# Kernel optimization log

Measured on AMD Instinct MI355X. Metric: run time of the kernel, lower is better.

Reference implementation:

```python
import jax, jax.numpy as jnp
import numpy as np

N, C, T, V = 64, 64, 128, 25
OUT, REL = 64, 8
MID = OUT // 2
BN_EPS = 1e-5


def _conv1x1(x, w, b):
    # 1x1 Conv2d: x [n,c,h,w_], w [o,c], b [o]
    return jnp.einsum('nchw,oc->nohw', x, w) + b[None, :, None, None]


def _forward(x, A, w1, b1, w2, b2, w11, b11, w22, b22, w3, b3, w4, b4,
             watt, batt, w5, b5, wc1, bc1, bn_g, bn_b, bn_m, bn_v,
             wc2, bc2, ws, bs, beita, alpha):
    T_ = x.shape[2]
    rel = w1.shape[0]
    x1 = _conv1x1(x, w1, b1)                          # [N,rel,T,V]
    x2 = _conv1x1(x, w2, b2)
    x1_mean, x2_mean = x1.mean(2), x2.mean(2)         # [N,rel,V]
    x1_max, x2_max = x1.max(2), x2.max(2)
    mean_res = x1_mean[:, :, :, None] - x2_mean[:, :, None, :]   # [N,rel,V,V]
    max_res = x1_max[:, :, :, None] - x2_max[:, :, None, :]
    # conv5: grouped 1x1 conv (groups=rel, 2 in-ch/group). The cat(dim=2)+reshape
    # interleaves channels as (mean[c], max[c]) pairs, so per-group it is:
    x_1 = jnp.tanh(w5[None, :, 0, None, None] * mean_res
                   + w5[None, :, 1, None, None] * max_res
                   + b5[None, :, None, None]) * alpha
    x_1 = _conv1x1(x_1, w4, b4)                       # [N,out,V,V]
    x3 = _conv1x1(x, w3, b3)                          # [N,out,T,V]
    x1_res = x_1 + A[None, None]
    # channel-wise spatial correlation attention
    att = jnp.tanh(jnp.einsum('nctu,nctv->ncuv', x1, x2) / T_)
    att = _conv1x1(att, watt, batt)                   # [N,out,V,V]
    global_res = jnp.einsum('nctu,ncuv->nctv', x3, att)
    # Bi_Inter 'channel': global avg pool -> 1x1 -> BN(inference) -> GELU -> 1x1 -> sigmoid
    g = global_res.mean((2, 3), keepdims=True)        # [N,out,1,1]
    h = _conv1x1(g, wc1, bc1)
    h = (h - bn_m[None, :, None, None]) * (bn_g[None, :, None, None]
        / jnp.sqrt(bn_v[None, :, None, None] + BN_EPS)) + bn_b[None, :, None, None]
    h = jax.nn.gelu(h, approximate=False)
    c_att = jax.nn.sigmoid(_conv1x1(h, wc2, bc2))     # [N,out,1,1]
    x1_res = c_att * x1_res
    x1_res = jnp.einsum('ncuv,nctv->nctu', x1_res, x3)  # [N,out,T,V]
    # Bi_Inter 'spatial': mean over T -> 1x1 (out->1) -> sigmoid
    s_att = jax.nn.sigmoid(_conv1x1(x1_res.mean(2, keepdims=True), ws, bs))  # [N,1,1,V]
    global_res = global_res * s_att
    x1_res = x1_res + global_res
    # per-frame spatial correlation (temporal branch)
    x11 = _conv1x1(x, w11, b11)
    x22 = _conv1x1(x, w22, b22)
    xt = jnp.tanh(jnp.einsum('nctv,nctu->ntvu', x11, x22) / rel)  # [N,T,V,V]
    t_res = jnp.einsum('nctu,ntuv->nctv', x3, xt)
    return t_res * beita + x1_res                     # [N,out,T,V]


def setup_inputs() -> dict:
    key = jax.random.key(0)
    ks = jax.random.split(key, 16)
    def nrm(i, shape, s=0.05):
        return jax.random.normal(ks[i], shape, jnp.float32) * s
    return {
        'x': jax.random.normal(ks[0], (N, C, T, V), jnp.float32),
        'A': nrm(1, (V, V), 0.1),
        'w1': nrm(2, (REL, C)), 'b1': jnp.zeros((REL,), jnp.float32),
        'w2': nrm(3, (REL, C)), 'b2': jnp.zeros((REL,), jnp.float32),
        'w11': nrm(4, (REL, C)), 'b11': jnp.zeros((REL,), jnp.float32),
        'w22': nrm(5, (REL, C)), 'b22': jnp.zeros((REL,), jnp.float32),
        'w3': nrm(6, (OUT, C)), 'b3': jnp.zeros((OUT,), jnp.float32),
        'w4': nrm(7, (OUT, REL)), 'b4': jnp.zeros((OUT,), jnp.float32),
        'watt': nrm(8, (OUT, REL)), 'batt': jnp.zeros((OUT,), jnp.float32),
        'w5': nrm(9, (REL, 2)), 'b5': jnp.zeros((REL,), jnp.float32),
        'wc1': nrm(10, (MID, OUT)), 'bc1': jnp.zeros((MID,), jnp.float32),
        'bn_g': jnp.ones((MID,), jnp.float32), 'bn_b': jnp.zeros((MID,), jnp.float32),
        'bn_m': jnp.zeros((MID,), jnp.float32), 'bn_v': jnp.ones((MID,), jnp.float32),
        'wc2': nrm(11, (OUT, MID)), 'bc2': jnp.zeros((OUT,), jnp.float32),
        'ws': nrm(12, (1, OUT)), 'bs': jnp.zeros((1,), jnp.float32),
        'beita': jnp.full((1,), 0.5, jnp.float32),
        'alpha': 1,
    }


def reference(x, A, w1, b1, w2, b2, w11, b11, w22, b22, w3, b3, w4, b4,
              watt, batt, w5, b5, wc1, bc1, bn_g, bn_b, bn_m, bn_v,
              wc2, bc2, ws, bs, beita, alpha):
    return _forward(x, A, w1, b1, w2, b2, w11, b11, w22, b22, w3, b3, w4, b4,
                    watt, batt, w5, b5, wc1, bc1, bn_g, bn_b, bn_m, bn_v,
                    wc2, bc2, ws, bs, beita, alpha)
```

## Files before the change

kernel.cpp:

```cpp
#include <hip/hip_runtime.h>
#include <hip/hip_bf16.h>
#include <math.h>

#define N_   64
#define C_   64
#define T_   128
#define V_   25
#define OUT_ 64
#define REL_ 8
#define MID_ 32
#define TV_  (T_*V_)
#define VV_  (V_*V_)
#define TT2  8
#define XTPF 28

typedef __hip_bfloat16 bf16;
typedef unsigned int uint;
typedef __attribute__((ext_vector_type(8))) short short8v;
typedef __attribute__((ext_vector_type(4))) float float4v;
__device__ __forceinline__ float b2f(bf16 x){ return __bfloat162float(x); }
__device__ __forceinline__ bf16  f2b(float x){ return __float2bfloat16(x); }
__device__ __forceinline__ float bfu(uint u){ return __uint_as_float(u<<16); }
__device__ __forceinline__ float bfh(uint u){ return __uint_as_float(u&0xffff0000u); }
__device__ __forceinline__ float bfs(unsigned short s){ return __uint_as_float(((uint)s)<<16); }

__device__ __forceinline__ float ftanh(float x){
    float cx = fminf(fmaxf(x, -15.f), 15.f);
    float e  = __expf(2.0f*cx);
    return (e - 1.0f) / (e + 1.0f);
}


__global__ __launch_bounds__(256) void k0_prep(
    const float* __restrict__ w1, const float* __restrict__ b1,
    const float* __restrict__ w2, const float* __restrict__ b2,
    const float* __restrict__ w11, const float* __restrict__ b11,
    const float* __restrict__ w22, const float* __restrict__ b22,
    const float* __restrict__ w3, const float* __restrict__ b3,
    unsigned short* __restrict__ WfragUS, float* __restrict__ Bg)
{
    int tid = threadIdx.x;
    for (int idx = tid; idx < 6144; idx += 256){
        int e  = idx & 7;
        int ln = (idx >> 3) & 63;
        int kb = (idx >> 9) & 1;
        int mt = idx >> 10;
        int m = mt*16 + (ln & 15);
        int k = kb*32 + ((ln >> 4) * 8) + e;
        float w;
        if      (m < 8)  w = w1[m*C_+k];
        else if (m < 16) w = w2[(m-8)*C_+k];
        else if (m < 24) w = w11[(m-16)*C_+k];
        else if (m < 32) w = w22[(m-24)*C_+k];
        else             w = w3[(m-32)*C_+k];
        bf16 h = f2b(w);
        WfragUS[idx] = *(unsigned short*)&h;
    }
    if (tid < 96){
        int o = tid; float bb;
        if      (o < 8)  bb = b1[o];
        else if (o < 16) bb = b2[o-8];
        else if (o < 24) bb = b11[o-16];
        else if (o < 32) bb = b22[o-24];
        else             bb = b3[o-32];
        Bg[o] = bb;
    }
}

__global__ __launch_bounds__(256) void k1_mfma(
    const float* __restrict__ x,
    const unsigned short* __restrict__ WfragUS, const float* __restrict__ Bg,
    bf16* __restrict__ x1h, bf16* __restrict__ x2h,
    bf16* __restrict__ x11h, bf16* __restrict__ x22h,
    bf16* __restrict__ x3h)
{
    __shared__ __align__(16) float xl[C_*64];
    __shared__ float Bl[96];
    int bid = blockIdx.x;
    int n = bid / 50, jt = bid % 50;
    int j0 = jt * 64;
    int tid = threadIdx.x;
    for (int e = tid; e < 1024; e += 256){
        int c = e >> 4, j4 = e & 15;
        ((float4*)xl)[e] = ((const float4*)(x + (size_t)(n*C_+c)*TV_ + j0))[j4];
    }
    if (tid < 96) Bl[tid] = Bg[tid];
    __syncthreads();

    int wave = tid >> 6, lane = tid & 63;
    int l15 = lane & 15, lg = lane >> 4;
    const short8v* wf = (const short8v*)WfragUS;
    short8v a[6][2];
    #pragma unroll
    for (int mt = 0; mt < 6; ++mt)
        #pragma unroll
        for (int kb = 0; kb < 2; ++kb)
            a[mt][kb] = wf[(mt*2 + kb)*64 + lane];
    int jw = wave*16 + l15;
    short8v b[2];
    #pragma unroll
    for (int kb = 0; kb < 2; ++kb){
        short8v bb;
        #pragma unroll
        for (int e = 0; e < 8; ++e){
            bf16 h = f2b(xl[(kb*32 + lg*8 + e)*64 + jw]);
            bb[e] = *(short*)&h;
        }
        b[kb] = bb;
    }
    float4v acc[6];
    #pragma unroll
    for (int mt = 0; mt < 6; ++mt) acc[mt] = (float4v){0.f,0.f,0.f,0.f};
    #pragma unroll
    for (int kb = 0; kb < 2; ++kb)
        #pragma unroll
        for (int mt = 0; mt < 6; ++mt)
            acc[mt] = __builtin_amdgcn_mfma_f32_16x16x32_bf16(a[mt][kb], b[kb], acc[mt], 0, 0, 0);

    int pos = j0 + jw;
    #pragma unroll
    for (int mt = 0; mt < 6; ++mt){
        #pragma unroll
        for (int reg = 0; reg < 4; ++reg){
            int o = mt*16 + lg*4 + reg;
            float val = acc[mt][reg] + Bl[o];
            bf16* dst = (o < 8)  ? x1h  + ((size_t)(n*REL_ + o     ))*TV_
                      : (o < 16) ? x2h  + ((size_t)(n*REL_ + o - 8 ))*TV_
                      : (o < 24) ? x11h + ((size_t)(n*REL_ + o - 16))*TV_
                      : (o < 32) ? x22h + ((size_t)(n*REL_ + o - 24))*TV_
                                 : x3h  + ((size_t)(n*OUT_ + o - 32))*TV_;
            dst[pos] = f2b(val);
        }
    }
}

__global__ __launch_bounds__(256) void k_x3bar2(const bf16* __restrict__ x3h,
                                                float* __restrict__ x3bar)
{
    __shared__ __align__(16) float xf[TV_];
    __shared__ float red[V_*8];
    int bid = blockIdx.x;
    int tid = threadIdx.x;
    for (int e = tid; e < 400; e += 256){
        uint4 p = ((const uint4*)(x3h + (size_t)bid*TV_))[e];
        float* d = xf + e*8;
        d[0]=bfu(p.x); d[1]=bfh(p.x); d[2]=bfu(p.y); d[3]=bfh(p.y);
        d[4]=bfu(p.z); d[5]=bfh(p.z); d[6]=bfu(p.w); d[7]=bfh(p.w);
    }
    __syncthreads();
    if (tid < 200){
        int v = tid % V_, g = tid / V_;
        float s = 0.f;
        #pragma unroll
        for (int k=0;k<16;++k) s += xf[(g*16+k)*V_ + v];
        red[g*V_+v] = s;
    }
    __syncthreads();
    if (tid < V_){
        float s = 0.f;
        #pragma unroll
        for (int g=0; g<8; ++g) s += red[g*V_+tid];
        x3bar[(size_t)bid*V_+tid] = s * (1.0f/T_);
    }
}

__global__ __launch_bounds__(256) void k3_mfma(
    const bf16* __restrict__ x1h, const bf16* __restrict__ x2h,
    const float* __restrict__ w5, const float* __restrict__ b5,
    const int* __restrict__ alpha,
    float* __restrict__ att8, float* __restrict__ xm)
{
    __shared__ __align__(16) unsigned short l1[TV_], l2[TV_];
    __shared__ float mu1l[V_], mu2l[V_], m1l[V_], m2l[V_];
    int bid = blockIdx.x;
    int tid = threadIdx.x;
    int r = bid % REL_;
    for (int e = tid; e < 400; e += 256){
        ((uint4*)l1)[e] = ((const uint4*)(x1h + (size_t)bid*TV_))[e];
        ((uint4*)l2)[e] = ((const uint4*)(x2h + (size_t)bid*TV_))[e];
    }
    __syncthreads();
    if (tid < 50){
        int v = tid % V_;
        const unsigned short* L = (tid < V_) ? l1 : l2;
        float s=0.f, mm=-1e30f;
        for (int t=0;t<T_;++t){
            float a = bfs(L[t*V_+v]);
            s += a; mm = fmaxf(mm, a);
        }
        if (tid < V_){ mu1l[v]=s*(1.0f/T_); m1l[v]=mm; }
        else         { mu2l[v]=s*(1.0f/T_); m2l[v]=mm; }
    }
    __syncthreads();
    int wave = tid >> 6, lane = tid & 63;
    int l15 = lane & 15, lg = lane >> 4;
    int mt = wave >> 1, nt = wave & 1;
    int mu = mt*16 + l15;
    int nv = nt*16 + l15;
    float4v acc = (float4v){0.f,0.f,0.f,0.f};
    #pragma unroll
    for (int kb = 0; kb < 4; ++kb){
        short8v av, bv;
        #pragma unroll
        for (int e = 0; e < 8; ++e){
            int k = kb*32 + lg*8 + e;
            av[e] = (mu < V_) ? (short)l1[k*V_ + mu] : (short)0;
            bv[e] = (nv < V_) ? (short)l2[k*V_ + nv] : (short)0;
        }
        acc = __builtin_amdgcn_mfma_f32_16x16x32_bf16(av, bv, acc, 0, 0, 0);
    }
    #pragma unroll
    for (int reg = 0; reg < 4; ++reg){
        int u = mt*16 + lg*4 + reg;
        if (u < V_ && nv < V_)
            att8[(size_t)bid*VV_ + u*V_ + nv] = ftanh(acc[reg]*(1.0f/T_));
    }
    float w50=w5[r*2+0], w51=w5[r*2+1], b5r=b5[r];
    float af = (float)alpha[0];
    for (int idx=tid; idx<VV_; idx+=256){
        int u = idx/V_, v = idx%V_;
        float mr = mu1l[u]-mu2l[v];
        float xr = m1l[u]-m2l[v];
        xm[(size_t)bid*VV_+idx] = ftanh(fmaf(w50,mr,fmaf(w51,xr,b5r))) * af;
    }
}

__global__ __launch_bounds__(256) void k6_chatt2(
    const float* __restrict__ att8, const float* __restrict__ x3bar,
    const float* __restrict__ watt, const float* __restrict__ batt,
    const float* __restrict__ wc1, const float* __restrict__ bc1,
    const float* __restrict__ bng, const float* __restrict__ bnb,
    const float* __restrict__ bnm, const float* __restrict__ bnv,
    const float* __restrict__ wc2, const float* __restrict__ bc2,
    float* __restrict__ catt)
{
    __shared__ float rs8[REL_*V_];
    __shared__ float gl[OUT_];
    __shared__ float hl[MID_];
    int n = blockIdx.x, tid = threadIdx.x;
    if (tid < REL_*V_){
        int r = tid / V_, u = tid % V_;
        const float* p = att8 + (size_t)(n*REL_+r)*VV_ + u*V_;
        float s = 0.f;
        #pragma unroll
        for (int v=0;v<V_;++v) s += p[v];
        rs8[tid] = s;
    }
    __syncthreads();
    if (tid < OUT_){
        int c = tid;
        const float* xb = x3bar + (size_t)(n*OUT_+c)*V_;
        float xbr[V_], sb = 0.f;
        #pragma unroll
        for (int u=0;u<V_;++u){ xbr[u]=xb[u]; sb += xbr[u]; }
        float s = 0.f;
        #pragma unroll
        for (int r=0;r<REL_;++r){
            float d = 0.f;
            #pragma unroll
            for (int u=0;u<V_;++u) d = fmaf(xbr[u], rs8[r*V_+u], d);
            s = fmaf(watt[c*REL_+r], d, s);
        }
        gl[c] = (s + (float)V_*batt[c]*sb) * (1.0f/(float)V_);
    }
    __syncthreads();
    if (tid < MID_){
        float h = bc1[tid];
        for (int c=0;c<OUT_;++c) h = fmaf(wc1[tid*OUT_+c], gl[c], h);
        h = (h - bnm[tid]) * bng[tid] * rsqrtf(bnv[tid] + 1e-5f) + bnb[tid];
        h = 0.5f*h*(1.0f+erff(h*0.70710678118654752f));
        hl[tid]=h;
    }
    __syncthreads();
    if (tid < OUT_){
        float s = bc2[tid];
        for (int m=0;m<MID_;++m) s = fmaf(wc2[tid*MID_+m], hl[m], s);
        catt[n*OUT_+tid] = 1.0f/(1.0f+expf(-s));
    }
}

__global__ __launch_bounds__(256) void k8_satt3(
    const float* __restrict__ xm, const float* __restrict__ A,
    const float* __restrict__ catt, const float* __restrict__ x3bar,
    const float* __restrict__ w4, const float* __restrict__ b4,
    const float* __restrict__ wsp, const float* __restrict__ bsp,
    float* __restrict__ satt)
{
    __shared__ __align__(16) float xml[REL_*VV_];
    __shared__ __align__(16) float xbl[OUT_*V_];
    __shared__ float Al[VV_];
    __shared__ float w4l[OUT_*REL_];
    __shared__ float scl[OUT_];
    __shared__ float Wl[REL_*V_];
    __shared__ float Yl[V_];
    __shared__ float red[OUT_];
    int n = blockIdx.x, tid = threadIdx.x;
    for (int e=tid; e<1250; e+=256)
        ((float4*)xml)[e] = ((const float4*)(xm + (size_t)n*REL_*VV_))[e];
    for (int e=tid; e<400; e+=256)
        ((float4*)xbl)[e] = ((const float4*)(x3bar + (size_t)n*OUT_*V_))[e];
    for (int e=tid; e<VV_; e+=256) Al[e] = A[e];
    for (int e=tid; e<OUT_*REL_; e+=256) w4l[e] = w4[e];
    if (tid < OUT_) scl[tid] = wsp[tid]*catt[n*OUT_+tid];
    __syncthreads();
    if (tid < REL_*V_){
        int r = tid/V_, v = tid%V_;
        float s = 0.f;
        for (int c=0;c<OUT_;++c) s = fmaf(scl[c]*w4l[c*REL_+r], xbl[c*V_+v], s);
        Wl[tid] = s;
    } else if (tid < REL_*V_ + V_){
        int v = tid - REL_*V_;
        float s = 0.f;
        for (int c=0;c<OUT_;++c) s = fmaf(scl[c], xbl[c*V_+v], s);
        Yl[v] = s;
    }
    __syncthreads();
    if (tid < OUT_){
        float s1 = 0.f;
        #pragma unroll
        for (int v=0;v<V_;++v) s1 += xbl[tid*V_+v];
        red[tid] = scl[tid]*b4[tid]*s1;
    }
    __syncthreads();
    if (tid < V_){
        int u = tid;
        float acc = 0.f;
        #pragma unroll
        for (int r=0;r<REL_;++r){
            const float* xr = xml + r*VV_ + u*V_;
            const float* wr = Wl + r*V_;
            #pragma unroll
            for (int v=0;v<V_;++v) acc = fmaf(xr[v], wr[v], acc);
        }
        #pragma unroll
        for (int v=0;v<V_;++v) acc = fmaf(Al[u*V_+v], Yl[v], acc);
        float beta = 0.f;
        for (int c=0;c<OUT_;++c) beta += red[c];
        satt[n*V_+u] = 1.0f/(1.0f+expf(-(bsp[0]+acc+beta)));
    }
}

__global__ __launch_bounds__(256) void k_comb3(
    const bf16* __restrict__ x3h,
    const float* __restrict__ att8, const float* __restrict__ xm,
    const float* __restrict__ A,
    const float* __restrict__ watt, const float* __restrict__ batt,
    const float* __restrict__ w4, const float* __restrict__ b4,
    const float* __restrict__ catt, const float* __restrict__ satt,
    bf16* __restrict__ combh)
{
    __shared__ __align__(16) unsigned short x3s[TV_];
    __shared__ float Ml[VV_];
    __shared__ float sl[V_];
    __shared__ __align__(16) unsigned short cst[TV_];
    int bid = blockIdx.x;
    int n = bid >> 6, c = bid & 63;
    int tid = threadIdx.x;
    for (int e = tid; e < 400; e += 256)
        ((uint4*)x3s)[e] = ((const uint4*)(x3h + (size_t)bid*TV_))[e];
    if (tid < V_) sl[tid] = satt[n*V_+tid];
    float ca = catt[bid];
    float w4r[REL_], war[REL_];
    #pragma unroll
    for (int r=0;r<REL_;++r){ w4r[r] = w4[c*REL_+r]; war[r] = watt[c*REL_+r]; }
    float b4c = b4[c], bac = batt[c];
    const float* xmn = xm  + (size_t)n*REL_*VV_;
    const float* a8n = att8 + (size_t)n*REL_*VV_;
    __syncthreads();
    for (int e = tid; e < VV_; e += 256){
        int w = e/V_, u = e%V_;
        float xv = b4c, av = bac;
        #pragma unroll
        for (int r=0;r<REL_;++r){
            xv = fmaf(w4r[r], xmn[r*VV_ + e], xv);
            av = fmaf(war[r], a8n[r*VV_ + u*V_ + w], av);
        }
        Ml[e] = ca*(xv + A[e]) + av*sl[w];
    }
    __syncthreads();
    int vh = tid & 1, tq = tid >> 1;
    int v0 = vh*13, nv = vh ? 12 : 13;
    float x3r[V_];
    #pragma unroll
    for (int u=0;u<V_;++u) x3r[u] = bfs(x3s[tq*V_+u]);
    for (int i=0;i<nv;++i){
        int v = v0+i;
        float s=0.f;
        #pragma unroll
        for (int u=0;u<V_;++u) s = fmaf(Ml[v*V_+u], x3r[u], s);
        bf16 h = f2b(s);
        cst[tq*V_+v] = *(unsigned short*)&h;
    }
    __syncthreads();
    for (int e = tid; e < 400; e += 256)
        ((uint4*)(combh + (size_t)bid*TV_))[e] = ((const uint4*)cst)[e];
}

__global__ __launch_bounds__(512) void k10_final8(
    const bf16* __restrict__ x11h, const bf16* __restrict__ x22h,
    const bf16* __restrict__ x3h, const bf16* __restrict__ combh,
    const float* __restrict__ beita, float* __restrict__ out)
{
    __shared__ __align__(16) char stg[25600];
    __shared__ __align__(16) float xtl[TT2*V_*XTPF];
    int bid = blockIdx.x;
    int n = bid >> 4, tt = bid & 15;
    int t0 = tt * TT2;
    int tid = threadIdx.x;
    float* l11 = (float*)stg;
    float* l22 = (float*)(stg + 6400);
    for (int e = tid; e < 400; e += 512){
        int half = (e >= 200);
        int i = half ? e-200 : e;
        int r = i / 25, ch = i % 25;
        const bf16* src = (half ? x22h : x11h) + (size_t)(n*REL_+r)*TV_ + t0*V_ + ch*8;
        uint4 p = *(const uint4*)src;
        float* d = (half ? l22 : l11) + i*8;
        d[0]=bfu(p.x); d[1]=bfh(p.x); d[2]=bfu(p.y); d[3]=bfh(p.y);
        d[4]=bfu(p.z); d[5]=bfh(p.z); d[6]=bfu(p.w); d[7]=bfh(p.w);
    }
    __syncthreads();
    for (int e = tid; e < TT2*VV_; e += 512){
        int ti = e / VV_, uv = e % VV_;
        int u = uv / V_, v = uv % V_;
        float s = 0.f;
        #pragma unroll
        for (int r = 0; r < REL_; ++r)
            s = fmaf(l11[r*200 + ti*V_ + u], l22[r*200 + ti*V_ + v], s);
        xtl[ti*(V_*XTPF) + u*XTPF + v] = ftanh(s * 0.125f);
    }
    float bt = beita[0];
    int vh = tid >> 8;
    int c_local = (tid >> 3) & 31;
    int ti = tid & 7;
    int vbase = vh ? 12 : 0;
    int nvv   = vh ? 13 : 12;
    for (int cr = 0; cr < 2; ++cr){
        int c0 = cr*32;
        __syncthreads();
        for (int e = tid; e < 1600; e += 512){
            int cl = e / 50, w = e % 50;
            size_t base = (size_t)(n*OUT_ + c0 + cl)*TV_ + (size_t)t0*V_;
            uint4 p = (w < 25) ? ((const uint4*)(combh + base))[w]
                               : ((const uint4*)(x3h  + base))[w-25];
            *(uint4*)(stg + cl*800 + (w<25 ? w*16 : 400 + (w-25)*16)) = p;
        }
        __syncthreads();
        const unsigned short* x3row = (const unsigned short*)(stg + c_local*800 + 400) + ti*V_;
        float acc[13];
        #pragma unroll
        for (int j=0;j<13;++j) acc[j]=0.f;
        const float* xbase = xtl + ti*(V_*XTPF) + vbase;
        #pragma unroll
        for (int u=0;u<V_;++u){
            float xa = bfs(x3row[u]);
            const float* xr = xbase + u*XTPF;
            if (vh == 0){
                #pragma unroll
                for (int j=0;j<12;++j) acc[j] = fmaf(xa, xr[j], acc[j]);
            } else {
                #pragma unroll
                for (int j=0;j<13;++j) acc[j] = fmaf(xa, xr[j], acc[j]);
            }
        }
        const unsigned short* cmbrow =
            (const unsigned short*)(stg + c_local*800) + ti*V_ + vbase;
        if (vh == 0){
            #pragma unroll
            for (int j=0;j<12;++j) acc[j] = fmaf(bt, acc[j], bfs(cmbrow[j]));
        } else {
            #pragma unroll
            for (int j=0;j<13;++j) acc[j] = fmaf(bt, acc[j], bfs(cmbrow[j]));
        }
        __syncthreads();
        float* orow = (float*)(stg + c_local*800 + ti*100) + vbase;
        if (vh == 0){
            #pragma unroll
            for (int j=0;j<12;++j) orow[j] = acc[j];
        } else {
            #pragma unroll
            for (int j=0;j<13;++j) orow[j] = acc[j];
        }
        __syncthreads();
        for (int e = tid; e < 1600; e += 512){
            int cl = e / 50, q = e % 50;
            *(float4*)(out + (size_t)(n*OUT_ + c0 + cl)*TV_ + (size_t)t0*V_ + q*4) =
                *(const float4*)(stg + cl*800 + q*16);
        }
    }
}

extern "C" void kernel_launch(void* const* d_in, const int* in_sizes, int n_in,
                              void* d_out, int out_size, void* d_ws, size_t ws_size,
                              hipStream_t stream)
{
    const float* x    = (const float*)d_in[0];
    const float* A    = (const float*)d_in[1];
    const float* w1   = (const float*)d_in[2];  const float* b1  = (const float*)d_in[3];
    const float* w2   = (const float*)d_in[4];  const float* b2  = (const float*)d_in[5];
    const float* w11  = (const float*)d_in[6];  const float* b11 = (const float*)d_in[7];
    const float* w22  = (const float*)d_in[8];  const float* b22 = (const float*)d_in[9];
    const float* w3   = (const float*)d_in[10]; const float* b3  = (const float*)d_in[11];
    const float* w4   = (const float*)d_in[12]; const float* b4  = (const float*)d_in[13];
    const float* watt = (const float*)d_in[14]; const float* batt= (const float*)d_in[15];
    const float* w5   = (const float*)d_in[16]; const float* b5  = (const float*)d_in[17];
    const float* wc1  = (const float*)d_in[18]; const float* bc1 = (const float*)d_in[19];
    const float* bng  = (const float*)d_in[20]; const float* bnb = (const float*)d_in[21];
    const float* bnm  = (const float*)d_in[22]; const float* bnv = (const float*)d_in[23];
    const float* wc2  = (const float*)d_in[24]; const float* bc2 = (const float*)d_in[25];
    const float* wsp  = (const float*)d_in[26]; const float* bsp = (const float*)d_in[27];
    const float* beita= (const float*)d_in[28];
    const int*  alpha = (const int*)d_in[29];
    float* out = (float*)d_out;

    char* wsb = (char*)d_ws;
    size_t off = 0;
    auto alloc = [&](size_t bytes)->char*{
        char* p = wsb + off;
        off += (bytes + 255) & ~(size_t)255;
        return p;
    };
    bf16*  x1h   = (bf16*) alloc((size_t)N_*REL_*TV_*2);
    bf16*  x2h   = (bf16*) alloc((size_t)N_*REL_*TV_*2);
    bf16*  x11h  = (bf16*) alloc((size_t)N_*REL_*TV_*2);
    bf16*  x22h  = (bf16*) alloc((size_t)N_*REL_*TV_*2);
    bf16*  x3h   = (bf16*) alloc((size_t)N_*OUT_*TV_*2);
    bf16*  combh = (bf16*) alloc((size_t)N_*OUT_*TV_*2);
    float* att8  = (float*)alloc((size_t)N_*REL_*VV_*4);
    float* xm    = (float*)alloc((size_t)N_*REL_*VV_*4);
    float* x3bar = (float*)alloc((size_t)N_*OUT_*V_*4);
    float* catt  = (float*)alloc((size_t)N_*OUT_*4);
    float* satt  = (float*)alloc((size_t)N_*V_*4);
    unsigned short* WfragUS = (unsigned short*)alloc((size_t)6144*2);
    float* Bg    = (float*)alloc((size_t)96*4);
    (void)ws_size; (void)n_in; (void)in_sizes; (void)out_size;

    k0_prep<<<1, 256, 0, stream>>>(w1,b1, w2,b2, w11,b11, w22,b22, w3,b3, WfragUS, Bg);
    k1_mfma<<<N_*50, 256, 0, stream>>>(x, WfragUS, Bg, x1h, x2h, x11h, x22h, x3h);
    k_x3bar2<<<N_*OUT_, 256, 0, stream>>>(x3h, x3bar);
    k3_mfma<<<N_*REL_, 256, 0, stream>>>(x1h, x2h, w5, b5, alpha, att8, xm);
    k6_chatt2<<<N_, 256, 0, stream>>>(att8, x3bar, watt, batt,
                                      wc1, bc1, bng, bnb, bnm, bnv, wc2, bc2, catt);
    k8_satt3<<<N_, 256, 0, stream>>>(xm, A, catt, x3bar, w4, b4, wsp, bsp, satt);
    k_comb3<<<N_*OUT_, 256, 0, stream>>>(x3h, att8, xm, A, watt, batt, w4, b4,
                                         catt, satt, combh);
    k10_final8<<<N_*16, 512, 0, stream>>>(x11h, x22h, x3h, combh, beita, out);
}
```

Measured before the change: 137.1 us.

## Split final stage into xt precompute kernel and MFMA-based output kernel

The per-timestep tanh(x11·x22) matrix is now computed by a separate kernel and written to global memory as bf16, laid out in MFMA fragment order and zero-padded to 32x32. The final kernel then loads these fragments and runs 16x16x32 bf16 MFMAs instead of scalar FMA loops, over twice as many blocks, each handling 32 channels. This removes the scalar FMA work and the fp32 xt tile in LDS. In exchange it adds an extra kernel launch, a global write and read of the xt buffer, and lowers xt to bf16 precision. Output stores are now scattered scalar writes instead of staged float4 writes.

```diff
diff --git a/kernel.cpp b/kernel.cpp
--- a/kernel.cpp
+++ b/kernel.cpp
@@ -12,7 +12,6 @@
 #define TV_  (T_*V_)
 #define VV_  (V_*V_)
 #define TT2  8
-#define XTPF 28
 
 typedef __hip_bfloat16 bf16;
 typedef unsigned int uint;
@@ -396,19 +395,16 @@
         ((uint4*)(combh + (size_t)bid*TV_))[e] = ((const uint4*)cst)[e];
 }
 
-__global__ __launch_bounds__(512) void k10_final8(
+__global__ __launch_bounds__(512) void k9_xt(
     const bf16* __restrict__ x11h, const bf16* __restrict__ x22h,
-    const bf16* __restrict__ x3h, const bf16* __restrict__ combh,
-    const float* __restrict__ beita, float* __restrict__ out)
-{
-    __shared__ __align__(16) char stg[25600];
-    __shared__ __align__(16) float xtl[TT2*V_*XTPF];
+    bf16* __restrict__ xtg)
+{
+    __shared__ __align__(16) float l11[REL_*TT2*V_];
+    __shared__ __align__(16) float l22[REL_*TT2*V_];
     int bid = blockIdx.x;
     int n = bid >> 4, tt = bid & 15;
     int t0 = tt * TT2;
     int tid = threadIdx.x;
-    float* l11 = (float*)stg;
-    float* l22 = (float*)(stg + 6400);
     for (int e = tid; e < 400; e += 512){
         int half = (e >= 200);
         int i = half ? e-200 : e;
@@ -420,72 +416,88 @@
         d[4]=bfu(p.z); d[5]=bfh(p.z); d[6]=bfu(p.w); d[7]=bfh(p.w);
     }
     __syncthreads();
-    for (int e = tid; e < TT2*VV_; e += 512){
-        int ti = e / VV_, uv = e % VV_;
-        int u = uv / V_, v = uv % V_;
-        float s = 0.f;
-        #pragma unroll
-        for (int r = 0; r < REL_; ++r)
-            s = fmaf(l11[r*200 + ti*V_ + u], l22[r*200 + ti*V_ + v], s);
-        xtl[ti*(V_*XTPF) + u*XTPF + v] = ftanh(s * 0.125f);
-    }
+    for (int idx = tid; idx < TT2*1024; idx += 512){
+        int ti  = idx >> 10;
+        int rem = idx & 1023;
+        int lane = (rem >> 3) & 63;
+        int e = rem & 7;
+        int u = ((lane >> 4) << 3) + e;
+        int v = ((rem >> 9) << 4) + (lane & 15);
+        float val = 0.f;
+        if (u < V_ && v < V_){
+            float s = 0.f;
+            #pragma unroll
+            for (int r = 0; r < REL_; ++r)
+                s = fmaf(l11[r*200 + ti*V_ + u], l22[r*200 + ti*V_ + v], s);
+            val = ftanh(s * 0.125f);
+        }
+        xtg[(size_t)(n*T_ + t0 + ti)*1024 + rem] = f2b(val);
+    }
+}
+
+__global__ __launch_bounds__(512) void k10_mfma(
+    const bf16* __restrict__ xtg,
+    const bf16* __restrict__ x3h, const bf16* __restrict__ combh,
+    const float* __restrict__ beita, float* __restrict__ out)
+{
+    __shared__ __align__(16) char stg[25600];
+    int bid = blockIdx.x;
+    int n = bid >> 5, rem = bid & 31;
+    int tt = rem >> 1, ch = rem & 1;
+    int t0 = tt * TT2, c0 = ch * 32;
+    int tid = threadIdx.x;
+    for (int e = tid; e < 1600; e += 512){
+        int cl = e / 50, w = e % 50;
+        size_t base = (size_t)(n*OUT_ + c0 + cl)*TV_ + (size_t)t0*V_;
+        uint4 p = (w < 25) ? ((const uint4*)(combh + base))[w]
+                           : ((const uint4*)(x3h  + base))[w-25];
+        *(uint4*)(stg + cl*800 + (w<25 ? w*16 : 400 + (w-25)*16)) = p;
+    }
+    __syncthreads();
     float bt = beita[0];
-    int vh = tid >> 8;
-    int c_local = (tid >> 3) & 31;
-    int ti = tid & 7;
-    int vbase = vh ? 12 : 0;
-    int nvv   = vh ? 13 : 12;
-    for (int cr = 0; cr < 2; ++cr){
-        int c0 = cr*32;
-        __syncthreads();
-        for (int e = tid; e < 1600; e += 512){
-            int cl = e / 50, w = e % 50;
-            size_t base = (size_t)(n*OUT_ + c0 + cl)*TV_ + (size_t)t0*V_;
-            uint4 p = (w < 25) ? ((const uint4*)(combh + base))[w]
-                               : ((const uint4*)(x3h  + base))[w-25];
-            *(uint4*)(stg + cl*800 + (w<25 ? w*16 : 400 + (w-25)*16)) = p;
-        }
-        __syncthreads();
-        const unsigned short* x3row = (const unsigned short*)(stg + c_local*800 + 400) + ti*V_;
-        float acc[13];
-        #pragma unroll
-        for (int j=0;j<13;++j) acc[j]=0.f;
-        const float* xbase = xtl + ti*(V_*XTPF) + vbase;
-        #pragma unroll
-        for (int u=0;u<V_;++u){
-            float xa = bfs(x3row[u]);
-            const float* xr = xbase + u*XTPF;
-            if (vh == 0){
-                #pragma unroll
-                for (int j=0;j<12;++j) acc[j] = fmaf(xa, xr[j], acc[j]);
-            } else {
-                #pragma unroll
-                for (int j=0;j<13;++j) acc[j] = fmaf(xa, xr[j], acc[j]);
+    int wave = tid >> 6, lane = tid & 63;
+    int ti = wave;
+    int t = t0 + ti;
+    int l15 = lane & 15, lg = lane >> 4;
+    const short8v* bp = (const short8v*)(xtg + (size_t)(n*T_ + t)*1024);
+    short8v bfr[2];
+    bfr[0] = bp[lane];
+    bfr[1] = bp[64 + lane];
+    short8v afr[2];
+    #pragma unroll
+    for (int mt = 0; mt < 2; ++mt){
+        short8v av;
+        #pragma unroll
+        for (int e = 0; e < 8; ++e){
+            int u = lg*8 + e;
+            int cl = mt*16 + l15;
+            av[e] = (u < V_) ? *(const short*)(stg + cl*800 + 400 + ti*50 + u*2)
+                             : (short)0;
+        }
+        afr[mt] = av;
+    }
+    float4v acc[2][2];
+    #pragma unroll
+    for (int mt = 0; mt < 2; ++mt)
+        #pragma unroll
+        for (int nt = 0; nt < 2; ++nt){
+            acc[mt][nt] = (float4v){0.f,0.f,0.f,0.f};
+            acc[mt][nt] = __builtin_amdgcn_mfma_f32_16x16x32_bf16(
+                              afr[mt], bfr[nt], acc[mt][nt], 0, 0, 0);
+        }
+    #pragma unroll
+    for (int mt = 0; mt < 2; ++mt){
+        #pragma unroll
+        for (int nt = 0; nt < 2; ++nt){
+            int v = nt*16 + l15;
+            if (v >= V_) continue;
+            #pragma unroll
+            for (int r = 0; r < 4; ++r){
+                int cl = mt*16 + lg*4 + r;
+                float cmb = bfs(*(const unsigned short*)(stg + cl*800 + ti*50 + v*2));
+                float val = fmaf(bt, acc[mt][nt][r], cmb);
+                out[(size_t)(n*OUT_ + c0 + cl)*TV_ + (size_t)t*V_ + v] = val;
             }
-        }
-        const unsigned short* cmbrow =
-            (const unsigned short*)(stg + c_local*800) + ti*V_ + vbase;
-        if (vh == 0){
-            #pragma unroll
-            for (int j=0;j<12;++j) acc[j] = fmaf(bt, acc[j], bfs(cmbrow[j]));
-        } else {
-            #pragma unroll
-            for (int j=0;j<13;++j) acc[j] = fmaf(bt, acc[j], bfs(cmbrow[j]));
-        }
-        __syncthreads();
-        float* orow = (float*)(stg + c_local*800 + ti*100) + vbase;
-        if (vh == 0){
-            #pragma unroll
-            for (int j=0;j<12;++j) orow[j] = acc[j];
-        } else {
-            #pragma unroll
-            for (int j=0;j<13;++j) orow[j] = acc[j];
-        }
-        __syncthreads();
-        for (int e = tid; e < 1600; e += 512){
-            int cl = e / 50, q = e % 50;
-            *(float4*)(out + (size_t)(n*OUT_ + c0 + cl)*TV_ + (size_t)t0*V_ + q*4) =
-                *(const float4*)(stg + cl*800 + q*16);
         }
     }
 }
@@ -526,6 +538,7 @@
     bf16*  x22h  = (bf16*) alloc((size_t)N_*REL_*TV_*2);
     bf16*  x3h   = (bf16*) alloc((size_t)N_*OUT_*TV_*2);
     bf16*  combh = (bf16*) alloc((size_t)N_*OUT_*TV_*2);
+    bf16*  xtg   = (bf16*) alloc((size_t)N_*T_*1024*2);
     float* att8  = (float*)alloc((size_t)N_*REL_*VV_*4);
     float* xm    = (float*)alloc((size_t)N_*REL_*VV_*4);
     float* x3bar = (float*)alloc((size_t)N_*OUT_*V_*4);
@@ -539,10 +552,11 @@
     k1_mfma<<<N_*50, 256, 0, stream>>>(x, WfragUS, Bg, x1h, x2h, x11h, x22h, x3h);
     k_x3bar2<<<N_*OUT_, 256, 0, stream>>>(x3h, x3bar);
     k3_mfma<<<N_*REL_, 256, 0, stream>>>(x1h, x2h, w5, b5, alpha, att8, xm);
+    k9_xt<<<N_*16, 512, 0, stream>>>(x11h, x22h, xtg);
     k6_chatt2<<<N_, 256, 0, stream>>>(att8, x3bar, watt, batt,
                                       wc1, bc1, bng, bnb, bnm, bnv, wc2, bc2, catt);
     k8_satt3<<<N_, 256, 0, stream>>>(xm, A, catt, x3bar, w4, b4, wsp, bsp, satt);
     k_comb3<<<N_*OUT_, 256, 0, stream>>>(x3h, att8, xm, A, watt, batt, w4, b4,
                                          catt, satt, combh);
-    k10_final8<<<N_*16, 512, 0, stream>>>(x11h, x22h, x3h, combh, beita, out);
-}
+    k10_mfma<<<N_*32, 512, 0, stream>>>(xtg, x3h, combh, beita, out);
+}
```

Result: faster. 133.9 us (-2.3%).
